# Kernel optimization log

Measured on AMD Instinct MI355X. Metric: run time of the kernel, lower is better.

Reference implementation:

```python
import jax, jax.numpy as jnp
import numpy as np

N_NODES = 25000
N_EDGES = 250000
F_IN = 32
F_OUT = 32
EDGE_DIM = 6
H1, H2 = 64, 128


def setup_inputs() -> dict:
    key = jax.random.key(0)
    ks = jax.random.split(key, 10)
    s = 0.05
    return {
        "x": jax.random.normal(ks[0], (N_NODES, F_IN), dtype=jnp.float32),
        "edge_attr": jax.random.normal(ks[1], (N_EDGES, EDGE_DIM), dtype=jnp.float32),
        # fnet MLP params: Linear(6->64), ReLU, Linear(64->128), ReLU, Linear(128->F_IN*F_OUT)
        "W1": jax.random.normal(ks[2], (H1, EDGE_DIM), dtype=jnp.float32) * s,
        "b1": jnp.zeros((H1,), dtype=jnp.float32),
        "W2": jax.random.normal(ks[3], (H2, H1), dtype=jnp.float32) * s,
        "b2": jnp.zeros((H2,), dtype=jnp.float32),
        "W3": jax.random.normal(ks[4], (F_IN * F_OUT, H2), dtype=jnp.float32) * s,
        "b3": jnp.zeros((F_IN * F_OUT,), dtype=jnp.float32),
        "edge_src": jax.random.randint(ks[5], (N_EDGES,), 0, N_NODES),
        "edge_dst": jax.random.randint(ks[6], (N_EDGES,), 0, N_NODES),
    }


def reference(x, edge_attr, W1, b1, W2, b2, W3, b3, edge_src, edge_dst):
    # fnet: per-edge MLP producing a dynamic filter theta_e of shape [F_OUT, F_IN]
    h = jax.nn.relu(edge_attr @ W1.T + b1)            # [E, H1]
    h = jax.nn.relu(h @ W2.T + b2)                    # [E, H2]
    theta = (h @ W3.T + b3).reshape(-1, F_OUT, F_IN)  # [E, F_OUT, F_IN]
    # gather source features, apply per-edge filter
    msg = jnp.einsum('eoi,ei->eo', theta, x[edge_src])  # [E, F_OUT]
    # scatter-mean over destination nodes (ECC averages over neighborhood)
    agg = jax.ops.segment_sum(msg, edge_dst, num_segments=N_NODES)
    deg = jax.ops.segment_sum(jnp.ones((msg.shape[0],), x.dtype), edge_dst,
                              num_segments=N_NODES)
    out = agg / jnp.maximum(deg, 1.0)[:, None]        # [N, F_OUT]
    return jax.nn.relu(out)                           # trailing 'r' in config
```

## Files before the change

### kernel.cpp

```cpp
#include <hip/hip_runtime.h>
#include <hip/hip_fp16.h>

#define N_NODES 25000
#define N_EDGES 250000
#define ED 6
#define H1 64
#define H2 128
#define NBLK 977
#define E_PAD (NBLK*256)
#define NCHUNK 33
#define CHUNK_USH 4096
#define W3S_USHORTS (NCHUNK*CHUNK_USH)
#define W2S_USHORTS (H2*H1)
#define SCAN_BLOCKS 98

typedef float f32x4 __attribute__((ext_vector_type(4)));
typedef float f32x16 __attribute__((ext_vector_type(16)));
typedef _Float16 f16x8 __attribute__((ext_vector_type(8)));
typedef __fp16 fp16x2 __attribute__((ext_vector_type(2)));
typedef unsigned int u32x4 __attribute__((ext_vector_type(4)));
typedef unsigned int u32x2 __attribute__((ext_vector_type(2)));

union F16x8U { u32x4 u; f16x8 h; };
union PKU    { fp16x2 p; unsigned u; };
union HU     { unsigned short u; _Float16 h; };

__device__ __forceinline__ unsigned pkrtz(float lo, float hi) {
    PKU r; r.p = __builtin_amdgcn_cvt_pkrtz(lo, hi); return r.u;
}
__device__ __forceinline__ unsigned pk_mul_blo(unsigned h, unsigned x) {
    unsigned d;
    asm("v_pk_mul_f16 %0, %1, %2 op_sel:[0,0] op_sel_hi:[0,1]" : "=v"(d) : "v"(h), "v"(x));
    return d;
}
__device__ __forceinline__ unsigned pk_mul_bhi(unsigned h, unsigned x) {
    unsigned d;
    asm("v_pk_mul_f16 %0, %1, %2 op_sel:[1,0] op_sel_hi:[1,1]" : "=v"(d) : "v"(h), "v"(x));
    return d;
}
__device__ __forceinline__ f32x4 mfma16(f16x8 a, f16x8 b, f32x4 c) {
    return __builtin_amdgcn_mfma_f32_16x16x32_f16(a, b, c, 0, 0, 0);
}
__device__ __forceinline__ f32x16 mfma32(f16x8 a, f16x8 b, f32x16 c) {
    return __builtin_amdgcn_mfma_f32_32x32x16_f16(a, b, c, 0, 0, 0);
}
__device__ __forceinline__ void gload16(const void* g, void* l) {
    __builtin_amdgcn_global_load_lds(
        (const __attribute__((address_space(1))) unsigned int*)g,
        (__attribute__((address_space(3))) unsigned int*)l, 16, 0, 0);
}

__global__ __launch_bounds__(256) void ecc_init(
    const float* __restrict__ W3, const float* __restrict__ b3,
    const float* __restrict__ W2,
    unsigned* __restrict__ cnt, unsigned short* __restrict__ w3s,
    unsigned short* __restrict__ w2s)
{
    int idx = blockIdx.x * 256 + threadIdx.x;
    if (idx < W3S_USHORTS) {
        int c = idx >> 12, r = idx & 4095;
        int ks = r >> 9;
        int lane = (r >> 3) & 63;
        int j = r & 7;
        int o = lane & 31;
        int kp = c * 128 + ks * 16 + ((lane >> 5) << 3) + j;
        float v = 0.f;
        if (kp < 4096)      { int k = kp >> 5, i = kp & 31; v = W3[(o * 32 + i) * 128 + k]; }
        else if (kp < 4128) { v = b3[o * 32 + (kp - 4096)]; }
        __half hv = __float2half_rn(v);
        w3s[idx] = *reinterpret_cast<unsigned short*>(&hv);
    }
    if (idx < W2S_USHORTS) {
        __half hv = __float2half_rn(W2[idx]);
        w2s[idx] = *reinterpret_cast<unsigned short*>(&hv);
    }
    if (idx < N_NODES) cnt[idx] = 0u;
}

__global__ __launch_bounds__(256) void ecc_hist(
    const int* __restrict__ dst, unsigned* __restrict__ cnt,
    unsigned* __restrict__ rank)
{
    int e = blockIdx.x * 256 + threadIdx.x;
    if (e < N_EDGES) rank[e] = atomicAdd(&cnt[dst[e]], 1u);
}

__global__ __launch_bounds__(256) void ecc_scan1(
    const unsigned* __restrict__ cnt, unsigned* __restrict__ off,
    unsigned* __restrict__ bsum)
{
    __shared__ unsigned s[256];
    const int t = threadIdx.x, i = blockIdx.x * 256 + t;
    unsigned v = (i < N_NODES) ? cnt[i] : 0u;
    s[t] = v; __syncthreads();
    #pragma unroll
    for (int d = 1; d < 256; d <<= 1) {
        unsigned add = (t >= d) ? s[t - d] : 0u;
        __syncthreads(); s[t] += add; __syncthreads();
    }
    if (i < N_NODES) off[i] = s[t] - v;
    if (t == 255) bsum[blockIdx.x] = s[255];
}

__global__ __launch_bounds__(128) void ecc_scan2(
    const unsigned* __restrict__ bsum, unsigned* __restrict__ bsumx)
{
    __shared__ unsigned s[128];
    const int t = threadIdx.x;
    unsigned v = (t < SCAN_BLOCKS) ? bsum[t] : 0u;
    s[t] = v; __syncthreads();
    #pragma unroll
    for (int d = 1; d < 128; d <<= 1) {
        unsigned add = (t >= d) ? s[t - d] : 0u;
        __syncthreads(); s[t] += add; __syncthreads();
    }
    if (t < SCAN_BLOCKS) bsumx[t] = s[t] - v;
}

__global__ __launch_bounds__(256) void ecc_scan3(
    unsigned* __restrict__ off, const unsigned* __restrict__ bsumx)
{
    int i = blockIdx.x * 256 + threadIdx.x;
    if (i < N_NODES) off[i] += bsumx[blockIdx.x];
    if (i == 0) off[N_NODES] = N_EDGES;
}

__global__ __launch_bounds__(256) void ecc_perm(
    const int* __restrict__ dst, const unsigned* __restrict__ off,
    const unsigned* __restrict__ rank, unsigned* __restrict__ perm)
{
    int e = blockIdx.x * 256 + threadIdx.x;
    if (e < N_EDGES) perm[off[dst[e]] + rank[e]] = (unsigned)e;
}

__global__ __launch_bounds__(256) void ecc_fused(
    const float* __restrict__ x,   const float* __restrict__ ea,
    const float* __restrict__ W1,  const float* __restrict__ b1,
    const unsigned short* __restrict__ w2s, const float* __restrict__ b2,
    const unsigned short* __restrict__ w3s,
    const int* __restrict__ src,   const unsigned* __restrict__ perm,
    unsigned short* __restrict__ msgT)
{
    __shared__ __align__(16) unsigned short sm[256 * H2];
    __shared__ __align__(16) unsigned short wbuf[2][CHUNK_USH];

    const int t = threadIdx.x;
    const int tile = blockIdx.x * 256;
    const int slot = tile + t;
    const bool ev = (slot < N_EDGES);
    const unsigned je = ev ? perm[slot] : 0u;

    const int w = t >> 6, l = t & 63, lr = l & 15, kg = l >> 4;
    const int l31 = l & 31, l5 = l >> 5;

    gload16(w3s + t * 8,        &wbuf[0][t * 8]);
    gload16(w3s + 2048 + t * 8, &wbuf[0][2048 + t * 8]);

    {
        float a[ED];
        #pragma unroll
        for (int c = 0; c < ED; ++c) a[c] = ev ? ea[(long)je * ED + c] : 0.f;

        float h1[H1];
        #pragma unroll
        for (int o = 0; o < H1; ++o) {
            float acc = b1[o];
            #pragma unroll
            for (int c = 0; c < ED; ++c) acc = fmaf(W1[o * ED + c], a[c], acc);
            h1[o] = fmaxf(acc, 0.f);
        }
        #pragma unroll
        for (int q = 0; q < 8; ++q) {
            u32x4 pk;
            #pragma unroll
            for (int j = 0; j < 4; ++j)
                pk[j] = pkrtz(h1[q*8 + 2*j], h1[q*8 + 2*j + 1]);
            const int boff = (t * 128 + q * 16) ^ ((t & 7) << 4);
            *(u32x4*)((char*)sm + boff) = pk;
        }
    }

    unsigned xsh[2][8];
    #pragma unroll
    for (int mt = 0; mt < 2; ++mt) {
        const int er = tile + w * 64 + mt * 32 + l31;
        if (er < N_EDGES) {
            const float* xb = x + (long)src[perm[er]] * 32;
            const float4* xp = (const float4*)(xb + l5 * 8);
            const float4* xq = (const float4*)(xb + 16 + l5 * 8);
            float4 v0 = xp[0], v1 = xp[1], v2 = xq[0], v3 = xq[1];
            xsh[mt][0] = pkrtz(v0.x, v0.y); xsh[mt][1] = pkrtz(v0.z, v0.w);
            xsh[mt][2] = pkrtz(v1.x, v1.y); xsh[mt][3] = pkrtz(v1.z, v1.w);
            xsh[mt][4] = pkrtz(v2.x, v2.y); xsh[mt][5] = pkrtz(v2.z, v2.w);
            xsh[mt][6] = pkrtz(v3.x, v3.y); xsh[mt][7] = pkrtz(v3.z, v3.w);
        } else {
            #pragma unroll
            for (int j = 0; j < 8; ++j) xsh[mt][j] = 0u;
        }
    }

    {
        F16x8U hb[4][2];
        #pragma unroll
        for (int ne = 0; ne < 4; ++ne) {
            const int er = w * 64 + ne * 16 + lr;
            #pragma unroll
            for (int ks = 0; ks < 2; ++ks) {
                const int boff = (er * 128 + ks * 64 + kg * 16) ^ ((er & 7) << 4);
                hb[ne][ks].u = *(const u32x4*)((const char*)sm + boff);
            }
        }
        __syncthreads();

        #pragma unroll
        for (int mo = 0; mo < 8; ++mo) {
            F16x8U a2[2];
            #pragma unroll
            for (int ks = 0; ks < 2; ++ks)
                a2[ks].u = *(const u32x4*)(w2s + (mo*16 + lr) * 64 + ks*32 + kg*8);
            const float4 bv = *(const float4*)(b2 + mo*16 + kg*4);
            #pragma unroll
            for (int ne = 0; ne < 4; ++ne) {
                f32x4 c = (f32x4){0.f, 0.f, 0.f, 0.f};
                c = mfma16(a2[0].h, hb[ne][0].h, c);
                c = mfma16(a2[1].h, hb[ne][1].h, c);
                const unsigned p0 = pkrtz(fmaxf(c[0]+bv.x, 0.f), fmaxf(c[1]+bv.y, 0.f));
                const unsigned p1 = pkrtz(fmaxf(c[2]+bv.z, 0.f), fmaxf(c[3]+bv.w, 0.f));
                const int er = w * 64 + ne * 16 + lr;
                const int boff = (er * 256 + (mo*16 + kg*4) * 2) ^ ((er & 7) << 4);
                *(u32x2*)((char*)sm + boff) = (u32x2){p0, p1};
            }
        }
    }

    f32x16 acc[2];
    #pragma unroll
    for (int i = 0; i < 16; ++i) { acc[0][i] = 0.f; acc[1][i] = 0.f; }

    __syncthreads();

    int cur = 0;
    #pragma unroll 1
    for (int c = 0; c < 32; ++c) {
        {
            const unsigned short* gs = w3s + (c + 1) * CHUNK_USH + t * 8;
            gload16(gs,        &wbuf[cur ^ 1][t * 8]);
            gload16(gs + 2048, &wbuf[cur ^ 1][2048 + t * 8]);
        }
        const char* wb = (const char*)wbuf[cur] + l * 16;

        u32x2 hv[2];
        #pragma unroll
        for (int mt = 0; mt < 2; ++mt) {
            const int row = w * 64 + mt * 32 + l31;
            const int boff = (row * 256 + c * 8) ^ ((row & 7) << 4);
            hv[mt] = *(const u32x2*)((const char*)sm + boff);
        }

        __builtin_amdgcn_s_setprio(1);
        #pragma unroll
        for (int ks = 0; ks < 8; ++ks) {
            F16x8U bf;
            bf.u = *(const u32x4*)(wb + ks * 1024);
            const int kl = ks >> 1;
            const int xb = (ks & 1) * 4;
            #pragma unroll
            for (int mt = 0; mt < 2; ++mt) {
                const unsigned h01 = hv[mt][kl >> 1];
                F16x8U af;
                if (kl & 1) {
                    af.u[0] = pk_mul_bhi(h01, xsh[mt][xb + 0]);
                    af.u[1] = pk_mul_bhi(h01, xsh[mt][xb + 1]);
                    af.u[2] = pk_mul_bhi(h01, xsh[mt][xb + 2]);
                    af.u[3] = pk_mul_bhi(h01, xsh[mt][xb + 3]);
                } else {
                    af.u[0] = pk_mul_blo(h01, xsh[mt][xb + 0]);
                    af.u[1] = pk_mul_blo(h01, xsh[mt][xb + 1]);
                    af.u[2] = pk_mul_blo(h01, xsh[mt][xb + 2]);
                    af.u[3] = pk_mul_blo(h01, xsh[mt][xb + 3]);
                }
                acc[mt] = mfma32(af.h, bf.h, acc[mt]);
            }
        }
        __builtin_amdgcn_s_setprio(0);

        __syncthreads();
        cur ^= 1;
    }
    {
        const char* wb = (const char*)wbuf[cur] + l * 16;
        F16x8U bf0, bf1;
        bf0.u = *(const u32x4*)(wb);
        bf1.u = *(const u32x4*)(wb + 1024);
        #pragma unroll
        for (int mt = 0; mt < 2; ++mt) {
            F16x8U af;
            af.u = (u32x4){xsh[mt][0], xsh[mt][1], xsh[mt][2], xsh[mt][3]};
            acc[mt] = mfma32(af.h, bf0.h, acc[mt]);
            af.u = (u32x4){xsh[mt][4], xsh[mt][5], xsh[mt][6], xsh[mt][7]};
            acc[mt] = mfma32(af.h, bf1.h, acc[mt]);
        }
    }

    {
        const long orow = (long)l31 * E_PAD;
        const int ebase = tile + w * 64 + 4 * l5;
        #pragma unroll
        for (int mt = 0; mt < 2; ++mt) {
            #pragma unroll
            for (int q = 0; q < 4; ++q) {
                const unsigned p0 = pkrtz(acc[mt][4*q + 0], acc[mt][4*q + 1]);
                const unsigned p1 = pkrtz(acc[mt][4*q + 2], acc[mt][4*q + 3]);
                const long e0 = ebase + mt * 32 + 8 * q;
                *(u32x2*)(msgT + orow + e0) = (u32x2){p0, p1};
            }
        }
    }
}

__global__ __launch_bounds__(256) void ecc_gather(
    const unsigned short* __restrict__ msgT, const unsigned* __restrict__ off,
    float* __restrict__ out)
{
    const int t = threadIdx.x;
    const int o = t & 31;
    const int n = blockIdx.x * 8 + (t >> 5);
    if (n >= N_NODES) return;
    const unsigned lo = off[n], hi = off[n + 1];
    const unsigned short* row = msgT + (long)o * E_PAD;
    float s = 0.f;
    for (unsigned j = lo; j < hi; ++j) {
        HU v; v.u = row[j];
        s += (float)v.h;
    }
    const float dg = fmaxf((float)(hi - lo), 1.f);
    out[(long)n * 32 + o] = fmaxf(s / dg, 0.f);
}

extern "C" void kernel_launch(void* const* d_in, const int* in_sizes, int n_in,
                              void* d_out, int out_size, void* d_ws, size_t ws_size,
                              hipStream_t stream) {
    const float* x   = (const float*)d_in[0];
    const float* ea  = (const float*)d_in[1];
    const float* W1  = (const float*)d_in[2];
    const float* b1  = (const float*)d_in[3];
    const float* W2  = (const float*)d_in[4];
    const float* b2  = (const float*)d_in[5];
    const float* W3  = (const float*)d_in[6];
    const float* b3  = (const float*)d_in[7];
    const int*   src = (const int*)d_in[8];
    const int*   dst = (const int*)d_in[9];
    float* out = (float*)d_out;

    char* p = (char*)d_ws;
    unsigned short* w3s = (unsigned short*)p; p += W3S_USHORTS * 2;
    unsigned short* w2s = (unsigned short*)p; p += 16384;
    unsigned* cnt   = (unsigned*)p; p += 100096;
    unsigned* off   = (unsigned*)p; p += 100352;
    unsigned* bsum  = (unsigned*)p; p += 512;
    unsigned* bsumx = (unsigned*)p; p += 512;
    unsigned* rank  = (unsigned*)p; p += 1000192;
    unsigned* perm  = (unsigned*)p; p += 1000192;
    unsigned short* msgT = (unsigned short*)p;

    ecc_init<<<(W3S_USHORTS + 255) / 256, 256, 0, stream>>>(W3, b3, W2, cnt, w3s, w2s);
    ecc_hist<<<NBLK, 256, 0, stream>>>(dst, cnt, rank);
    ecc_scan1<<<SCAN_BLOCKS, 256, 0, stream>>>(cnt, off, bsum);
    ecc_scan2<<<1, 128, 0, stream>>>(bsum, bsumx);
    ecc_scan3<<<SCAN_BLOCKS, 256, 0, stream>>>(off, bsumx);
    ecc_perm<<<NBLK, 256, 0, stream>>>(dst, off, rank, perm);
    ecc_fused<<<NBLK, 256, 0, stream>>>(x, ea, W1, b1, w2s, b2, w3s, src, perm, msgT);
    ecc_gather<<<(N_NODES + 7) / 8, 256, 0, stream>>>(msgT, off, out);
}
```

Baseline: 136.7 us.

## Fuse segment reduction into the edge kernel using shared-memory partial sums and atomics

Result: slower. 171.4 us (+25.4%).

```diff
diff --git a/kernel.cpp b/kernel.cpp
--- a/kernel.cpp
+++ b/kernel.cpp
@@ -7,7 +7,6 @@
 #define H1 64
 #define H2 128
 #define NBLK 977
-#define E_PAD (NBLK*256)
 #define NCHUNK 33
 #define CHUNK_USH 4096
 #define W3S_USHORTS (NCHUNK*CHUNK_USH)
@@ -77,6 +76,11 @@
     if (idx < N_NODES) cnt[idx] = 0u;
 }
 
+__global__ __launch_bounds__(256) void ecc_zero_agg(float* __restrict__ agg) {
+    int i = blockIdx.x * 256 + threadIdx.x;
+    if (i < N_NODES * 32) agg[i] = 0.f;
+}
+
 __global__ __launch_bounds__(256) void ecc_hist(
     const int* __restrict__ dst, unsigned* __restrict__ cnt,
     unsigned* __restrict__ rank)
@@ -139,10 +143,11 @@
     const unsigned short* __restrict__ w2s, const float* __restrict__ b2,
     const unsigned short* __restrict__ w3s,
     const int* __restrict__ src,   const unsigned* __restrict__ perm,
-    unsigned short* __restrict__ msgT)
+    const unsigned* __restrict__ off, float* __restrict__ agg)
 {
     __shared__ __align__(16) unsigned short sm[256 * H2];
     __shared__ __align__(16) unsigned short wbuf[2][CHUNK_USH];
+    __shared__ int n0s;
 
     const int t = threadIdx.x;
     const int tile = blockIdx.x * 256;
@@ -155,6 +160,15 @@
 
     gload16(w3s + t * 8,        &wbuf[0][t * 8]);
     gload16(w3s + 2048 + t * 8, &wbuf[0][2048 + t * 8]);
+
+    if (t == 0) {
+        int loN = 0, hiN = N_NODES;
+        while (loN < hiN) {
+            int mid = (loN + hiN) >> 1;
+            if (off[mid + 1] > (unsigned)tile) hiN = mid; else loN = mid + 1;
+        }
+        n0s = loN;
+    }
 
     {
         float a[ED];
@@ -302,39 +316,54 @@
         }
     }
 
+    __syncthreads();
     {
-        const long orow = (long)l31 * E_PAD;
-        const int ebase = tile + w * 64 + 4 * l5;
+        unsigned short* msgl = (unsigned short*)sm;
         #pragma unroll
         for (int mt = 0; mt < 2; ++mt) {
             #pragma unroll
-            for (int q = 0; q < 4; ++q) {
-                const unsigned p0 = pkrtz(acc[mt][4*q + 0], acc[mt][4*q + 1]);
-                const unsigned p1 = pkrtz(acc[mt][4*q + 2], acc[mt][4*q + 3]);
-                const long e0 = ebase + mt * 32 + 8 * q;
-                *(u32x2*)(msgT + orow + e0) = (u32x2){p0, p1};
+            for (int rg = 0; rg < 16; ++rg) {
+                const int el = w * 64 + mt * 32 + (rg & 3) + 8 * (rg >> 2) + 4 * l5;
+                HU hv; hv.h = (_Float16)acc[mt][rg];
+                msgl[el * 32 + l31] = hv.u;
             }
         }
     }
-}
-
-__global__ __launch_bounds__(256) void ecc_gather(
-    const unsigned short* __restrict__ msgT, const unsigned* __restrict__ off,
+    __syncthreads();
+
+    {
+        const unsigned short* msgl = (const unsigned short*)sm;
+        const int n0 = n0s;
+        const int tend = tile + 256;
+        #pragma unroll 1
+        for (int p = t; ; p += 256) {
+            const int n = n0 + (p >> 5);
+            if (n >= N_NODES) break;
+            const unsigned lo = off[n], hi = off[n + 1];
+            if ((int)lo >= tend) break;
+            const int o = p & 31;
+            const int jb = max((int)lo, tile), jend = min((int)hi, tend);
+            if (jend > jb) {
+                float s = 0.f;
+                for (int j = jb; j < jend; ++j) {
+                    HU v; v.u = msgl[(j - tile) * 32 + o];
+                    s += (float)v.h;
+                }
+                atomicAdd(&agg[(long)n * 32 + o], s);
+            }
+        }
+    }
+}
+
+__global__ __launch_bounds__(256) void ecc_finalize(
+    const float* __restrict__ agg, const unsigned* __restrict__ cnt,
     float* __restrict__ out)
 {
-    const int t = threadIdx.x;
-    const int o = t & 31;
-    const int n = blockIdx.x * 8 + (t >> 5);
-    if (n >= N_NODES) return;
-    const unsigned lo = off[n], hi = off[n + 1];
-    const unsigned short* row = msgT + (long)o * E_PAD;
-    float s = 0.f;
-    for (unsigned j = lo; j < hi; ++j) {
-        HU v; v.u = row[j];
-        s += (float)v.h;
-    }
-    const float dg = fmaxf((float)(hi - lo), 1.f);
-    out[(long)n * 32 + o] = fmaxf(s / dg, 0.f);
+    const int i = blockIdx.x * 256 + threadIdx.x;
+    if (i >= N_NODES * 32) return;
+    const int n = i >> 5;
+    const float d = fmaxf((float)cnt[n], 1.f);
+    out[i] = fmaxf(agg[i] / d, 0.f);
 }
 
 extern "C" void kernel_launch(void* const* d_in, const int* in_sizes, int n_in,
@@ -361,14 +390,15 @@
     unsigned* bsumx = (unsigned*)p; p += 512;
     unsigned* rank  = (unsigned*)p; p += 1000192;
     unsigned* perm  = (unsigned*)p; p += 1000192;
-    unsigned short* msgT = (unsigned short*)p;
+    float*    agg   = (float*)p;
 
     ecc_init<<<(W3S_USHORTS + 255) / 256, 256, 0, stream>>>(W3, b3, W2, cnt, w3s, w2s);
+    ecc_zero_agg<<<(N_NODES * 32 + 255) / 256, 256, 0, stream>>>(agg);
     ecc_hist<<<NBLK, 256, 0, stream>>>(dst, cnt, rank);
     ecc_scan1<<<SCAN_BLOCKS, 256, 0, stream>>>(cnt, off, bsum);
     ecc_scan2<<<1, 128, 0, stream>>>(bsum, bsumx);
     ecc_scan3<<<SCAN_BLOCKS, 256, 0, stream>>>(off, bsumx);
     ecc_perm<<<NBLK, 256, 0, stream>>>(dst, off, rank, perm);
-    ecc_fused<<<NBLK, 256, 0, stream>>>(x, ea, W1, b1, w2s, b2, w3s, src, perm, msgT);
-    ecc_gather<<<(N_NODES + 7) / 8, 256, 0, stream>>>(msgT, off, out);
-}
+    ecc_fused<<<NBLK, 256, 0, stream>>>(x, ea, W1, b1, w2s, b2, w3s, src, perm, off, agg);
+    ecc_finalize<<<(N_NODES * 32 + 255) / 256, 256, 0, stream>>>(agg, cnt, out);
+}
```
